# Kernel tuning notes

Measured on AMD Instinct MI355X. Metric: run time of the kernel, lower is better.

## Reference

```python
import jax, jax.numpy as jnp
import numpy as np
from jax import lax

D_MODEL = 768
N_LAYERS = 2
D_STATE = 16
D_CONV = 4
EXPAND = 2
D_INNER = EXPAND * D_MODEL
DT_RANK = 48  # ceil(768/16)
BETA = 0.9
ALPHA = 1.0
NS_STEPS = 1
EPS = 1e-5
BATCH = 2
SEQ = 512


def rmsnorm(x, w):
    return x * lax.rsqrt(jnp.mean(x * x, axis=-1, keepdims=True) + EPS) * w


def newton_schulz(X, steps):
    # Muon quintic Newton-Schulz orthogonalization on (B, D_INNER, D_STATE) matrices.
    a, b, c = 3.4445, -4.7750, 2.0315
    G = jnp.swapaxes(X, -1, -2)  # (B, N, Di) rows < cols
    G = G / (jnp.sqrt(jnp.sum(G * G, axis=(-2, -1), keepdims=True)) + 1e-7)
    for _ in range(steps):
        A = G @ jnp.swapaxes(G, -1, -2)  # (B, N, N)
        G = a * G + (b * A + c * (A @ A)) @ G
    return jnp.swapaxes(G, -1, -2)


def mamba_mixer(x, in_w, cw, cb, xp_w, dtp_w, dtp_b, A_log, Dp, out_w):
    B_, L, _ = x.shape
    xz = jnp.einsum('bld,ed->ble', x, in_w)  # (B, L, 2*Di)
    xi, z = jnp.split(xz, 2, axis=-1)
    # causal depthwise conv1d + silu
    xc = lax.conv_general_dilated(
        jnp.swapaxes(xi, 1, 2), cw, window_strides=(1,),
        padding=[(D_CONV - 1, 0)],
        dimension_numbers=('NCH', 'OIH', 'NCH'),
        feature_group_count=D_INNER)
    xc = jax.nn.silu(jnp.swapaxes(xc, 1, 2) + cb)  # (B, L, Di)
    x_dbl = jnp.einsum('bld,ed->ble', xc, xp_w)
    dt_lr = x_dbl[..., :DT_RANK]
    Bm = x_dbl[..., DT_RANK:DT_RANK + D_STATE]  # (B, L, N)
    Cm = x_dbl[..., DT_RANK + D_STATE:]         # (B, L, N)
    dt = jax.nn.softplus(jnp.einsum('blr,dr->bld', dt_lr, dtp_w) + dtp_b)
    A = -jnp.exp(A_log)  # (Di, N)
    dA = jnp.exp(dt[..., None] * A)                            # (B, L, Di, N)
    dBx = dt[..., None] * Bm[:, :, None, :] * xc[..., None]    # (B, L, Di, N)

    def step(carry, inp):
        h, v = carry
        dA_t, dBx_t, C_t = inp
        v = BETA * v + dBx_t                 # momentum velocity
        vu = newton_schulz(v, NS_STEPS)      # NS-orthogonalized update
        h = dA_t * h + ALPHA * vu
        y = jnp.einsum('bdn,bn->bd', h, C_t)
        return (h, v), y

    h0 = jnp.zeros((B_, D_INNER, D_STATE), x.dtype)
    v0 = jnp.zeros_like(h0)
    xs = (jnp.moveaxis(dA, 1, 0), jnp.moveaxis(dBx, 1, 0), jnp.moveaxis(Cm, 1, 0))
    _, ys = lax.scan(step, (h0, v0), xs)
    y = jnp.moveaxis(ys, 0, 1) + Dp * xc
    y = y * jax.nn.silu(z)
    return jnp.einsum('bld,ed->ble', y, out_w)


def forward(x, in_proj_w, conv_w, conv_b, x_proj_w, dt_proj_w, dt_proj_b,
            A_log, D, out_proj_w, norm_w, final_norm_w):
    for i in range(N_LAYERS):
        x = mamba_mixer(rmsnorm(x, norm_w[i]), in_proj_w[i], conv_w[i], conv_b[i],
                        x_proj_w[i], dt_proj_w[i], dt_proj_b[i], A_log[i], D[i],
                        out_proj_w[i]) + x
    return rmsnorm(x, final_norm_w)


def setup_inputs() -> dict:
    key = jax.random.key(0)
    ks = jax.random.split(key, 8)
    s = 0.02
    scale_out = s / np.sqrt(2 * N_LAYERS)
    A_init = jnp.broadcast_to(jnp.arange(1, D_STATE + 1, dtype=jnp.float32), (N_LAYERS, D_INNER, D_STATE))
    return {
        'x': jax.random.normal(ks[0], (BATCH, SEQ, D_MODEL), jnp.float32),
        'in_proj_w': jax.random.normal(ks[1], (N_LAYERS, 2 * D_INNER, D_MODEL), jnp.float32) * s,
        'conv_w': jax.random.normal(ks[2], (N_LAYERS, D_INNER, 1, D_CONV), jnp.float32) * 0.5,
        'conv_b': jnp.zeros((N_LAYERS, D_INNER), jnp.float32),
        'x_proj_w': jax.random.normal(ks[3], (N_LAYERS, DT_RANK + 2 * D_STATE, D_INNER), jnp.float32) * s,
        'dt_proj_w': jax.random.normal(ks[4], (N_LAYERS, D_INNER, DT_RANK), jnp.float32) * (DT_RANK ** -0.5),
        'dt_proj_b': jax.random.uniform(ks[5], (N_LAYERS, D_INNER), jnp.float32, -4.0, -2.0),
        'A_log': jnp.log(A_init),
        'D': jnp.ones((N_LAYERS, D_INNER), jnp.float32),
        'out_proj_w': jax.random.normal(ks[6], (N_LAYERS, D_MODEL, D_INNER), jnp.float32) * scale_out,
        'norm_w': jnp.ones((N_LAYERS, D_MODEL), jnp.float32),
        'final_norm_w': jnp.ones((D_MODEL,), jnp.float32),
    }


def reference(x, in_proj_w, conv_w, conv_b, x_proj_w, dt_proj_w, dt_proj_b,
              A_log, D, out_proj_w, norm_w, final_norm_w):
    return forward(x, in_proj_w, conv_w, conv_b, x_proj_w, dt_proj_w, dt_proj_b,
                   A_log, D, out_proj_w, norm_w, final_norm_w)
```

## Files before the change

### kernel.cpp

```cpp
#include <hip/hip_runtime.h>
#include <math.h>

#define DM   768
#define DI   1536
#define NDS  16
#define DTR  48
#define XDC  80
#define XPN  128
#define NB   2
#define SEQL 512
#define NT   (NB*SEQL)
#define CC   32
#define TT   16
#define BETA 0.9f
#define NSA  3.4445f
#define NSB  (-4.775f)
#define NSC  2.0315f
#define LOG2E 1.4426950408889634f
#define GKH  768
#define GKS  772
#define NCOL 32

typedef __attribute__((ext_vector_type(8))) short short8v;
typedef __attribute__((ext_vector_type(4))) float f32x4;

__device__ __forceinline__ float silu_(float x){ return x / (1.f + __expf(-x)); }
__device__ __forceinline__ unsigned short bfr(float x){
  unsigned u = __float_as_uint(x);
  return (unsigned short)((u + 0x7fffu + ((u>>16)&1u)) >> 16);
}
__device__ __forceinline__ void gl_lds16(const unsigned short* g, unsigned short* l){
  __builtin_amdgcn_global_load_lds((const __attribute__((address_space(1))) void*)g,
                                   (__attribute__((address_space(3))) void*)l, 16, 0, 0);
}

__global__ void rms_k(const float* __restrict__ X, const float* __restrict__ W,
                      unsigned short* __restrict__ O)
{
  const int g = blockIdx.x, tid = threadIdx.x;
  const float* xr = X + (size_t)g*DM;
  float x0 = xr[tid], x1 = xr[tid+256], x2 = xr[tid+512];
  float ss = x0*x0 + x1*x1 + x2*x2;
  #pragma unroll
  for (int m=1; m<=32; m<<=1) ss += __shfl_xor(ss, m);
  __shared__ float ws[4];
  if ((tid & 63) == 0) ws[tid>>6] = ss;
  __syncthreads();
  float sc = rsqrtf((ws[0]+ws[1]+ws[2]+ws[3])*(1.f/DM) + 1e-5f);
  unsigned short* o = O + (size_t)g*DM;
  o[tid]     = bfr(x0*sc*W[tid]);
  o[tid+256] = bfr(x1*sc*W[tid+256]);
  o[tid+512] = bfr(x2*sc*W[tid+512]);
}

__global__ void castall_k(const float* __restrict__ in_w, const float* __restrict__ out_w,
                          const float* __restrict__ xp_w,
                          unsigned short* __restrict__ wIn, unsigned short* __restrict__ wOut,
                          unsigned short* __restrict__ wXp)
{
  const int T0 = 2*2*DI*DM/4, T1 = 2*DM*DI/4, T2 = 2*XPN*DI/4;
  int i = blockIdx.x*256 + threadIdx.x;
  if (i < T0){
    float4 v = ((const float4*)in_w)[i];
    ushort4 o = { bfr(v.x), bfr(v.y), bfr(v.z), bfr(v.w) };
    ((ushort4*)wIn)[i] = o;
    return;
  }
  i -= T0;
  if (i < T1){
    float4 v = ((const float4*)out_w)[i];
    ushort4 o = { bfr(v.x), bfr(v.y), bfr(v.z), bfr(v.w) };
    ((ushort4*)wOut)[i] = o;
    return;
  }
  i -= T1;
  if (i < T2){
    const int l = i / (XPN*DI/4);
    const int r = i % (XPN*DI/4);
    const int row = r / (DI/4);
    const int k4 = r % (DI/4);
    ushort4 o = {0,0,0,0};
    if (row < XDC){
      float4 v = *(const float4*)(xp_w + ((size_t)l*XDC + row)*DI + k4*4);
      o.x = bfr(v.x); o.y = bfr(v.y); o.z = bfr(v.z); o.w = bfr(v.w);
    }
    ((ushort4*)wXp)[i] = o;
  }
}

__global__ __launch_bounds__(256) void gemm_mf(
    const unsigned short* __restrict__ Abf, int lda,
    const unsigned short* __restrict__ Bbf, int ldb,
    float* __restrict__ Out, float* __restrict__ Part,
    int M, int N, int K, int SK)
{
  __shared__ unsigned short As[128*32];
  __shared__ unsigned short Bs[128*32];
  const int tid  = threadIdx.x;
  const int wid  = tid >> 6, lane = tid & 63;
  const int bm   = blockIdx.y*128, bn = blockIdx.x*128;
  const int kc   = K/SK, kBeg = blockIdx.z*kc, kEnd = kBeg + kc;
  const int wr   = (wid>>1)*64, wc = (wid&1)*64;

  f32x4 acc[4][4];
  #pragma unroll
  for (int m=0;m<4;m++)
    #pragma unroll
    for (int n=0;n<4;n++) acc[m][n] = (f32x4){0.f,0.f,0.f,0.f};

  const int e0 = (wid*2)*512 + lane*8;
  const int e1 = e0 + 512;
  const int r0 = e0 >> 5, k0e = e0 & 31;
  const int r1 = e1 >> 5, k1e = e1 & 31;
  const unsigned short* Ag0 = Abf + (size_t)(bm + r0)*lda + k0e;
  const unsigned short* Ag1 = Abf + (size_t)(bm + r1)*lda + k1e;
  const unsigned short* Bg0 = Bbf + (size_t)(bn + r0)*ldb + k0e;
  const unsigned short* Bg1 = Bbf + (size_t)(bn + r1)*ldb + k1e;

  int aoff[4], boff[4];
  #pragma unroll
  for (int m=0;m<4;m++) aoff[m] = (wr + m*16 + (lane&15))*32 + (lane>>4)*8;
  #pragma unroll
  for (int n=0;n<4;n++) boff[n] = (wc + n*16 + (lane&15))*32 + (lane>>4)*8;

  for (int k0 = kBeg; k0 < kEnd; k0 += 32){
    gl_lds16(Ag0 + k0, As + e0);
    gl_lds16(Ag1 + k0, As + e1);
    gl_lds16(Bg0 + k0, Bs + e0);
    gl_lds16(Bg1 + k0, Bs + e1);
    __syncthreads();
    short8v af[4], bfv[4];
    #pragma unroll
    for (int m=0;m<4;m++) af[m]  = *(const short8v*)(As + aoff[m]);
    #pragma unroll
    for (int n=0;n<4;n++) bfv[n] = *(const short8v*)(Bs + boff[n]);
    #pragma unroll
    for (int m=0;m<4;m++)
      #pragma unroll
      for (int n=0;n<4;n++)
        acc[m][n] = __builtin_amdgcn_mfma_f32_16x16x32_bf16(af[m], bfv[n], acc[m][n], 0, 0, 0);
    __syncthreads();
  }

  #pragma unroll
  for (int m=0;m<4;m++){
    const int rowb = bm + wr + m*16 + (lane>>4)*4;
    #pragma unroll
    for (int n=0;n<4;n++){
      const int col = bn + wc + n*16 + (lane&15);
      #pragma unroll
      for (int r=0;r<4;r++){
        const int row = rowb + r;
        if (SK == 1) Out[(size_t)row*N + col] = acc[m][n][r];
        else         Part[(size_t)blockIdx.z*M*N + (size_t)row*N + col] = acc[m][n][r];
      }
    }
  }
}

__global__ void gemm64w(const float* __restrict__ A, int lda,
                        const float* __restrict__ Bw, int ldb,
                        float* __restrict__ Out, float* __restrict__ wOut,
                        const float* __restrict__ bias, const float* __restrict__ xc,
                        int M, int N, int K)
{
  __shared__ float As[16][64], Bs[16][64];
  const int tid = threadIdx.x;
  const int bm = blockIdx.y*64, bn = blockIdx.x*64;
  const int lr = tid>>2, lk = (tid&3)<<2;
  const int tx = tid&15, ty = tid>>4;
  float acc[4][4];
  #pragma unroll
  for (int i=0;i<4;i++)
    #pragma unroll
    for (int j=0;j<4;j++) acc[i][j] = 0.f;
  const float* Ap = A + (size_t)(bm+lr)*lda + lk;
  const float* Bp = Bw + (size_t)(bn+lr)*ldb + lk;
  for (int k0=0; k0<K; k0+=16){
    float4 a0 = *(const float4*)(Ap + k0);
    float4 b0 = *(const float4*)(Bp + k0);
    __syncthreads();
    As[lk+0][lr]=a0.x; As[lk+1][lr]=a0.y; As[lk+2][lr]=a0.z; As[lk+3][lr]=a0.w;
    Bs[lk+0][lr]=b0.x; Bs[lk+1][lr]=b0.y; Bs[lk+2][lr]=b0.z; Bs[lk+3][lr]=b0.w;
    __syncthreads();
    #pragma unroll
    for (int kk=0;kk<16;kk++){
      float a[4], b[4];
      *(float4*)a = *(const float4*)&As[kk][ty*4];
      *(float4*)b = *(const float4*)&Bs[kk][tx*4];
      #pragma unroll
      for (int i=0;i<4;i++)
        #pragma unroll
        for (int j=0;j<4;j++) acc[i][j] = fmaf(a[i], b[j], acc[i][j]);
    }
  }
  #pragma unroll
  for (int i=0;i<4;i++){
    const int row = bm + ty*4 + i;
    #pragma unroll
    for (int j=0;j<4;j++){
      const int col = bn + tx*4 + j;
      float vv = acc[i][j] + bias[col];
      vv = fmaxf(vv,0.f) + log1pf(__expf(-fabsf(vv)));
      Out[(size_t)row*N+col]  = vv;
      wOut[(size_t)row*N+col] = vv * xc[(size_t)row*N+col];
    }
  }
}

__global__ void reducepad_k(const float* __restrict__ Part, float* __restrict__ Out)
{
  const int i = blockIdx.x*256 + threadIdx.x;
  if (i >= NT*XDC) return;
  const int row = i / XDC, col = i % XDC;
  float s = 0.f;
  #pragma unroll
  for (int z=0; z<8; z++) s += Part[(size_t)z*NT*XPN + (size_t)row*XPN + col];
  Out[i] = s;
}

template<int MODE>
__global__ void reduce_rms_k(const float* __restrict__ Part, const float* __restrict__ res,
                             const float* __restrict__ W, float* __restrict__ nxt,
                             unsigned short* __restrict__ xnb, float* __restrict__ dout)
{
  const int g = blockIdx.x, tid = threadIdx.x;
  float s[3];
  #pragma unroll
  for (int j=0;j<3;j++){
    const int e = tid + j*256;
    float v = res[(size_t)g*DM + e];
    #pragma unroll
    for (int z=0;z<4;z++) v += Part[(size_t)z*NT*DM + (size_t)g*DM + e];
    s[j] = v;
    if (MODE==1) nxt[(size_t)g*DM + e] = v;
  }
  float ss = s[0]*s[0] + s[1]*s[1] + s[2]*s[2];
  #pragma unroll
  for (int m=1; m<=32; m<<=1) ss += __shfl_xor(ss, m);
  __shared__ float ws[4];
  if ((tid & 63) == 0) ws[tid>>6] = ss;
  __syncthreads();
  float sc = rsqrtf((ws[0]+ws[1]+ws[2]+ws[3])*(1.f/DM) + 1e-5f);
  #pragma unroll
  for (int j=0;j<3;j++){
    const int e = tid + j*256;
    if (MODE==1) xnb[(size_t)g*DM + e] = bfr(s[j]*sc*W[e]);
    else         dout[(size_t)g*DM + e] = s[j]*sc*W[e];
  }
}

__global__ void conv_k(const float* __restrict__ xz, const float* __restrict__ cw,
                       const float* __restrict__ cb, float* __restrict__ xc,
                       unsigned short* __restrict__ xc16)
{
  const int d = blockIdx.x*256 + threadIdx.x;
  const int g = blockIdx.y;
  const int b = g >> 9, t = g & (SEQL-1);
  float4 w4 = *(const float4*)(cw + (size_t)d*4);
  const float wk[4] = {w4.x, w4.y, w4.z, w4.w};
  const float* col = xz + ((size_t)b*SEQL)*(2*DI) + d;
  float acc = cb[d];
  #pragma unroll
  for (int k=0;k<4;k++){
    int tt = t - 3 + k;
    if (tt >= 0) acc = fmaf(wk[k], col[(size_t)tt*(2*DI)], acc);
  }
  const float r = silu_(acc);
  xc[(size_t)g*DI + d]   = r;
  xc16[(size_t)g*DI + d] = bfr(r);
}

__global__ void vagg_k(const float* __restrict__ dt, const float* __restrict__ wb,
                       const float* __restrict__ xdbl, float* __restrict__ Vagg,
                       float* __restrict__ cumdt)
{
  const int d = blockIdx.x*256 + threadIdx.x;
  const int c = blockIdx.y, b = blockIdx.z;
  float acc[16];
  #pragma unroll
  for (int n=0;n<16;n++) acc[n] = 0.f;
  float sdt = 0.f;
  for (int s=0;s<TT;s++){
    const int g = b*SEQL + c*TT + s;
    sdt += dt[(size_t)g*DI + d];
    cumdt[(size_t)g*DI + d] = sdt;
    const float w = wb[(size_t)g*DI + d];
    #pragma unroll
    for (int n=0;n<16;n++) acc[n] = fmaf(BETA, acc[n], w * xdbl[(size_t)g*XDC + 48 + n]);
  }
  const size_t base = ((size_t)(b*CC + c)*NDS)*DI + d;
  #pragma unroll
  for (int n=0;n<16;n++) Vagg[base + (size_t)n*DI] = acc[n];
}

__global__ void vcomb_k(float* V, float betaT)
{
  const int d = blockIdx.x*256 + threadIdx.x;
  const int n = blockIdx.y, b = blockIdx.z;
  const size_t stride = (size_t)NDS*DI;
  size_t idx = ((size_t)(b*CC)*NDS + n)*DI + d;
  float a = V[idx];
  float v = 0.f;
  for (int c=0;c<CC;c++){
    float an = (c+1<CC) ? V[idx+stride] : 0.f;
    V[idx] = v;
    v = fmaf(betaT, v, a);
    a = an; idx += stride;
  }
}

__global__ __launch_bounds__(256) void gram_k(
    const float* __restrict__ vst, const float* __restrict__ wb,
    const float* __restrict__ xdbl, float* __restrict__ Qg)
{
  const int c = blockIdx.x, b = blockIdx.y;
  const int tid = threadIdx.x;
  __shared__ float Xs[NCOL*GKS];
  __shared__ float Ms[NCOL][NCOL+1];
  __shared__ float sB[TT][16];
  __shared__ float Rm[16][17];

  const size_t vbase = ((size_t)(b*CC + c)*NDS)*DI;
  const size_t gbase = (size_t)(b*SEQL + c*TT);

  const bool active = tid < 216;
  const int tile = tid / 6, seg = tid % 6;
  int ti = 0, tj = 0;
  {
    int tt = tile;
    if (active){ while (tt >= 8 - ti){ tt -= 8 - ti; ti++; } tj = ti + tt; }
  }
  const int i0 = ti*4, j0 = tj*4;
  const int ks = seg*128;
  float acc[4][4];
  #pragma unroll
  for (int i=0;i<4;i++)
    #pragma unroll
    for (int j=0;j<4;j++) acc[i][j] = 0.f;

  for (int pass = 0; pass < 2; pass++){
    const int koff = pass * GKH;
    __syncthreads();
    #pragma unroll
    for (int q = 0; q < 24; q++){
      const int p = tid + q*256;
      const int col = p / 192;
      const int kk  = (p % 192) * 4;
      float4 xv;
      if (col < 16) xv = *(const float4*)(vst + vbase + (size_t)col*DI + koff + kk);
      else          xv = *(const float4*)(wb + (gbase + (col-16))*DI + koff + kk);
      *(float4*)(Xs + col*GKS + kk) = xv;
    }
    __syncthreads();
    if (active){
      for (int k4 = 0; k4 < 128; k4 += 4){
        float4 av[4], bv[4];
        #pragma unroll
        for (int r=0;r<4;r++) av[r] = *(const float4*)(Xs + (i0+r)*GKS + ks + k4);
        #pragma unroll
        for (int r=0;r<4;r++) bv[r] = *(const float4*)(Xs + (j0+r)*GKS + ks + k4);
        #pragma unroll
        for (int i=0;i<4;i++)
          #pragma unroll
          for (int j=0;j<4;j++){
            float s = fmaf(av[i].x, bv[j].x, acc[i][j]);
            s = fmaf(av[i].y, bv[j].y, s);
            s = fmaf(av[i].z, bv[j].z, s);
            acc[i][j] = fmaf(av[i].w, bv[j].w, s);
          }
      }
    }
  }
  __syncthreads();
  if (active){
    #pragma unroll
    for (int e=0;e<16;e++) Xs[(tile*16 + e)*6 + seg] = acc[e>>2][e&3];
  }
  { const int s = tid>>4, n = tid&15; sB[s][n] = xdbl[(gbase + s)*XDC + 48 + n]; }
  __syncthreads();
  for (int o = tid; o < 576; o += 256){
    const int tl = o >> 4, e = o & 15;
    int tt = tl, ti2 = 0;
    while (tt >= 8 - ti2){ tt -= 8 - ti2; ti2++; }
    const int tj2 = ti2 + tt;
    const int i = ti2*4 + (e>>2), j = tj2*4 + (e&3);
    float s = 0.f;
    #pragma unroll
    for (int sg=0; sg<6; sg++) s += Xs[o*6 + sg];
    Ms[i][j] = s; Ms[j][i] = s;
  }
  __syncthreads();

  const int i = tid >> 4, j = tid & 15;
  float Rreg = Ms[i][j];
  constexpr float PB[17] = {1.f, 0.9f, 0.81f, 0.729f, 0.6561f, 0.59049f,
                            0.531441f, 0.4782969f, 0.43046721f, 0.387420489f,
                            0.3486784401f, 0.31381059609f, 0.282429536481f,
                            0.2541865828329f, 0.22876792454961f, 0.205891132094649f,
                            0.1853020188851841f};
  const size_t qbase = ((size_t)(b*CC + c)*TT)*256;
  #pragma unroll
  for (int t=0;t<TT;t++){
    float p_i = PB[t]*Ms[i][16+t];
    float p_j = PB[t]*Ms[j][16+t];
    #pragma unroll
    for (int r=0;r<t;r++){
      const float gg = Ms[16+r][16+t];
      p_i = fmaf(PB[t-1-r]*gg, sB[r][i], p_i);
      p_j = fmaf(PB[t-1-r]*gg, sB[r][j], p_j);
    }
    const float bi = sB[t][i], bj = sB[t][j];
    const float gtt = Ms[16+t][16+t];
    Rreg = BETA*BETA*Rreg + BETA*(p_i*bj + bi*p_j) + gtt*bi*bj;
    Rm[i][j] = Rreg;
    __syncthreads();
    float tr = 0.f;
    #pragma unroll
    for (int k=0;k<16;k++) tr += Rm[k][k];
    const float nu = sqrtf(tr) + 1e-7f;
    const float inv_nu = 1.f/nu;
    const float inv2 = inv_nu*inv_nu;
    const float inv4 = inv2*inv2;
    float a2v = 0.f;
    #pragma unroll
    for (int k=0;k<16;k++) a2v = fmaf(Rm[i][k], Rm[k][j], a2v);
    float q = NSB*inv2*Rreg + NSC*inv4*a2v;
    if (i == j) q += NSA;
    Qg[qbase + t*256 + tid] = q * inv_nu;
    __syncthreads();
  }
}

__global__ __launch_bounds__(256) void apply_k(
    float* vh, const float* __restrict__ dt,
    const float* __restrict__ wb, const float* __restrict__ xdbl,
    const float* __restrict__ Qg, const float* __restrict__ A_log,
    float* __restrict__ ylocal)
{
  const int c = blockIdx.x, b = blockIdx.y, z = blockIdx.z;
  const int tid = threadIdx.x;
  const int d = z*256 + tid;
  __shared__ float sQ[TT*256];
  __shared__ float sBC[TT][32];

  const size_t qbase = ((size_t)(b*CC + c)*TT)*256;
  #pragma unroll
  for (int q=0;q<TT;q++) sQ[q*256 + tid] = Qg[qbase + q*256 + tid];
  #pragma unroll
  for (int rr=0; rr<2; rr++){
    const int p = tid + rr*256;
    sBC[p>>5][p&31] = xdbl[(size_t)((size_t)b*SEQL + c*TT + (p>>5))*XDC + 48 + (p&31)];
  }
  __syncthreads();

  float v[16], h[16], Ar[16];
  {
    float* vs = vh + ((size_t)(b*CC + c)*NDS)*DI + d;
    const float* arow = A_log + (size_t)d*NDS;
    #pragma unroll
    for (int n=0;n<16;n++){
      v[n] = vs[(size_t)n*DI];
      h[n] = 0.f;
      Ar[n] = -__expf(arow[n]) * LOG2E;
    }
  }

  for (int t=0;t<TT;t++){
    const size_t g = (size_t)(b*SEQL + c*TT + t);
    const float dtv = dt[g*DI + d];
    const float wv  = wb[g*DI + d];
    #pragma unroll
    for (int n=0;n<16;n++) v[n] = fmaf(BETA, v[n], wv*sBC[t][n]);
    float un[16];
    #pragma unroll
    for (int n=0;n<16;n++) un[n] = 0.f;
    const float* qt = sQ + t*256;
    #pragma unroll
    for (int k=0;k<16;k++){
      const float vk = v[k];
      const float4 q0 = *(const float4*)(qt + k*16);
      const float4 q1 = *(const float4*)(qt + k*16 + 4);
      const float4 q2 = *(const float4*)(qt + k*16 + 8);
      const float4 q3 = *(const float4*)(qt + k*16 + 12);
      un[0]=fmaf(vk,q0.x,un[0]); un[1]=fmaf(vk,q0.y,un[1]); un[2]=fmaf(vk,q0.z,un[2]); un[3]=fmaf(vk,q0.w,un[3]);
      un[4]=fmaf(vk,q1.x,un[4]); un[5]=fmaf(vk,q1.y,un[5]); un[6]=fmaf(vk,q1.z,un[6]); un[7]=fmaf(vk,q1.w,un[7]);
      un[8]=fmaf(vk,q2.x,un[8]); un[9]=fmaf(vk,q2.y,un[9]); un[10]=fmaf(vk,q2.z,un[10]); un[11]=fmaf(vk,q2.w,un[11]);
      un[12]=fmaf(vk,q3.x,un[12]); un[13]=fmaf(vk,q3.y,un[13]); un[14]=fmaf(vk,q3.z,un[14]); un[15]=fmaf(vk,q3.w,un[15]);
    }
    float y = 0.f;
    #pragma unroll
    for (int n=0;n<16;n++){
      const float e = exp2f(dtv*Ar[n]);
      h[n] = fmaf(e, h[n], un[n]);
      y = fmaf(h[n], sBC[t][16+n], y);
    }
    ylocal[g*DI + d] = y;
  }
  float* he = vh + ((size_t)(b*CC + c)*NDS)*DI + d;
  #pragma unroll
  for (int n=0;n<16;n++) he[(size_t)n*DI] = h[n];
}

__global__ void hcomb_k(float* H, const float* __restrict__ cumdt,
                        const float* __restrict__ A_log)
{
  const int d = blockIdx.x*256 + threadIdx.x;
  const int n = blockIdx.y, b = blockIdx.z;
  const float An = -__expf(A_log[(size_t)d*NDS + n]);
  const size_t stride = (size_t)NDS*DI;
  const size_t sstep = (size_t)TT*DI;
  size_t idx  = ((size_t)(b*CC)*NDS + n)*DI + d;
  size_t sidx = ((size_t)b*SEQL + TT-1)*DI + d;
  float a = H[idx];
  float sv = cumdt[sidx];
  float hv = 0.f;
  for (int c=0;c<CC;c++){
    float an = 0.f, sn = 0.f;
    if (c+1 < CC){ an = H[idx+stride]; sn = cumdt[sidx+sstep]; }
    H[idx] = hv;
    hv = fmaf(__expf(An * sv), hv, a);
    a = an; sv = sn;
    idx += stride; sidx += sstep;
  }
}

__global__ void yepi_k(const float* __restrict__ ylocal, const float* __restrict__ hst,
                       const float* __restrict__ cumdt, const float* __restrict__ xdbl,
                       const float* __restrict__ A_log, const float* __restrict__ Dv,
                       const float* __restrict__ xcp, const float* __restrict__ xz,
                       unsigned short* __restrict__ ybf)
{
  const int d = blockIdx.x*256 + threadIdx.x;
  const int g = blockIdx.y;
  const int b = g >> 9, t = g & (SEQL-1);
  const int c = t / TT;
  const float ddt = cumdt[(size_t)g*DI + d];
  const float* hs = hst + ((size_t)(b*CC + c)*NDS)*DI + d;
  const float* ar = A_log + (size_t)d*NDS;
  float corr = 0.f;
  #pragma unroll
  for (int n=0;n<16;n++){
    float An = -__expf(ar[n]);
    float Cn = xdbl[(size_t)g*XDC + 64 + n];
    corr = fmaf(hs[(size_t)n*DI] * __expf(An*ddt), Cn, corr);
  }
  float y = ylocal[(size_t)g*DI + d] + corr + Dv[d]*xcp[(size_t)g*DI + d];
  float z = xz[(size_t)g*(2*DI) + DI + d];
  ybf[(size_t)g*DI + d] = bfr(y * silu_(z));
}

extern "C" void kernel_launch(void* const* d_in, const int* in_sizes, int n_in,
                              void* d_out, int out_size, void* d_ws, size_t ws_size,
                              hipStream_t stream)
{
  (void)in_sizes; (void)n_in; (void)out_size; (void)ws_size;
  const float* x      = (const float*)d_in[0];
  const float* in_w   = (const float*)d_in[1];
  const float* conv_w = (const float*)d_in[2];
  const float* conv_b = (const float*)d_in[3];
  const float* xp_w   = (const float*)d_in[4];
  const float* dtp_w  = (const float*)d_in[5];
  const float* dtp_b  = (const float*)d_in[6];
  const float* A_log  = (const float*)d_in[7];
  const float* Dp     = (const float*)d_in[8];
  const float* out_w  = (const float*)d_in[9];
  const float* norm_w = (const float*)d_in[10];
  const float* fnorm  = (const float*)d_in[11];

  const float betaT = powf(BETA, (float)TT);

  float* w0 = (float*)d_ws; size_t off = 0;
  auto alloc = [&](size_t n)->float*{ float* p = w0 + off; off += (n + 63) & ~(size_t)63; return p; };
  float* xa     = alloc((size_t)NT*DM);
  float* bfA    = alloc((size_t)NT*DI/2);
  float* xz     = alloc((size_t)NT*2*DI);
  float* xcb    = alloc((size_t)NT*DI);
  float* xcbbF  = alloc((size_t)NT*DI/2);
  float* xdbl   = alloc((size_t)NT*XDC);
  float* dtb    = alloc((size_t)NT*DI);
  float* wbuf   = alloc((size_t)NT*DI);
  float* cumdt  = alloc((size_t)NT*DI);
  float* ylocal = alloc((size_t)NT*DI);
  float* Qg     = alloc((size_t)NB*CC*TT*256);
  float* big1   = alloc((size_t)NB*CC*NDS*DI);
  float* partb  = alloc((size_t)4*NT*DM);
  float* wInF   = alloc((size_t)2*2*DI*DM/2);
  float* wOutF  = alloc((size_t)2*DM*DI/2);
  float* wXpF   = alloc((size_t)2*XPN*DI/2);

  unsigned short* xnb  = (unsigned short*)bfA;
  unsigned short* ybf  = (unsigned short*)bfA;
  unsigned short* xcbb = (unsigned short*)xcbbF;
  unsigned short* wInb = (unsigned short*)wInF;
  unsigned short* wOutb= (unsigned short*)wOutF;
  unsigned short* wXpb = (unsigned short*)wXpF;

  {
    const int T0 = 2*2*DI*DM/4, T1 = 2*DM*DI/4, T2 = 2*XPN*DI/4;
    castall_k<<<dim3((T0+T1+T2+255)/256), dim3(256), 0, stream>>>(
        in_w, out_w, xp_w, wInb, wOutb, wXpb);
  }
  rms_k<<<dim3(NT), dim3(256), 0, stream>>>(x, norm_w, xnb);

  const float* xcur = x;
  for (int l=0; l<2; l++){
    const unsigned short* wIn_l  = wInb  + (size_t)l*2*DI*DM;
    const unsigned short* wOut_l = wOutb + (size_t)l*DM*DI;
    const unsigned short* wXp_l  = wXpb  + (size_t)l*XPN*DI;
    const float* cw_l  = conv_w + (size_t)l*DI*4;
    const float* cb_l  = conv_b + (size_t)l*DI;
    const float* dtw_l = dtp_w  + (size_t)l*DI*DTR;
    const float* dtbi  = dtp_b  + (size_t)l*DI;
    const float* al_l  = A_log  + (size_t)l*DI*NDS;
    const float* d_l   = Dp     + (size_t)l*DI;

    gemm_mf<<<dim3(2*DI/128, NT/128, 1), dim3(256), 0, stream>>>(
        xnb, DM, wIn_l, DM, xz, nullptr, NT, 2*DI, DM, 1);
    conv_k<<<dim3(DI/256, NT), dim3(256), 0, stream>>>(xz, cw_l, cb_l, xcb, xcbb);
    gemm_mf<<<dim3(XPN/128, NT/128, 8), dim3(256), 0, stream>>>(
        xcbb, DI, wXp_l, DI, nullptr, partb, NT, XPN, DI, 8);
    reducepad_k<<<dim3((NT*XDC+255)/256), dim3(256), 0, stream>>>(partb, xdbl);
    gemm64w<<<dim3(DI/64, NT/64, 1), dim3(256), 0, stream>>>(
        xdbl, XDC, dtw_l, DTR, dtb, wbuf, dtbi, xcb, NT, DI, DTR);
    vagg_k<<<dim3(DI/256, CC, NB), dim3(256), 0, stream>>>(dtb, wbuf, xdbl, big1, cumdt);
    vcomb_k<<<dim3(DI/256, NDS, NB), dim3(256), 0, stream>>>(big1, betaT);
    gram_k<<<dim3(CC, NB), dim3(256), 0, stream>>>(big1, wbuf, xdbl, Qg);
    apply_k<<<dim3(CC, NB, DI/256), dim3(256), 0, stream>>>(
        big1, dtb, wbuf, xdbl, Qg, al_l, ylocal);
    hcomb_k<<<dim3(DI/256, NDS, NB), dim3(256), 0, stream>>>(big1, cumdt, al_l);
    yepi_k<<<dim3(DI/256, NT), dim3(256), 0, stream>>>(
        ylocal, big1, cumdt, xdbl, al_l, d_l, xcb, xz, ybf);
    gemm_mf<<<dim3(DM/128, NT/128, 4), dim3(256), 0, stream>>>(
        ybf, DI, wOut_l, DI, nullptr, partb, NT, DM, DI, 4);
    if (l == 0)
      reduce_rms_k<1><<<dim3(NT), dim3(256), 0, stream>>>(
          partb, xcur, norm_w + DM, xa, xnb, nullptr);
    else
      reduce_rms_k<2><<<dim3(NT), dim3(256), 0, stream>>>(
          partb, xcur, fnorm, nullptr, nullptr, (float*)d_out);
    xcur = xa;
  }
}
```

Before: 441.9 us.

## Halve scan chunk length and fuse silu(z) into in_proj GEMM epilogue

Shrinks the chunked momentum-scan chunk from 16 to 8 timesteps (64 chunks), retuning the Gram kernel's tiling, thread mapping and shared-memory arrays to match, so per-chunk Gram and apply work is smaller and more parallel. Separately, the in_proj GEMM epilogue now writes x fp32 and silu(z) as bf16 into split buffers, so the z half no longer round-trips through the fp32 buffer and yepi reads half the bytes. The trade-offs are more chunks to combine sequentially in vcomb/hcomb, and slightly less precision on the gate.

```diff
diff --git a/kernel.cpp b/kernel.cpp
--- a/kernel.cpp
+++ b/kernel.cpp
@@ -10,8 +10,8 @@
 #define NB   2
 #define SEQL 512
 #define NT   (NB*SEQL)
-#define CC   32
-#define TT   16
+#define CC   64
+#define TT   8
 #define BETA 0.9f
 #define NSA  3.4445f
 #define NSB  (-4.775f)
@@ -19,7 +19,6 @@
 #define LOG2E 1.4426950408889634f
 #define GKH  768
 #define GKS  772
-#define NCOL 32
 
 typedef __attribute__((ext_vector_type(8))) short short8v;
 typedef __attribute__((ext_vector_type(4))) float f32x4;
@@ -28,6 +27,9 @@
 __device__ __forceinline__ unsigned short bfr(float x){
   unsigned u = __float_as_uint(x);
   return (unsigned short)((u + 0x7fffu + ((u>>16)&1u)) >> 16);
+}
+__device__ __forceinline__ float bf2f(unsigned short u){
+  return __uint_as_float(((unsigned)u) << 16);
 }
 __device__ __forceinline__ void gl_lds16(const unsigned short* g, unsigned short* l){
   __builtin_amdgcn_global_load_lds((const __attribute__((address_space(1))) void*)g,
@@ -88,10 +90,12 @@
   }
 }
 
+template<int EPI>
 __global__ __launch_bounds__(256) void gemm_mf(
     const unsigned short* __restrict__ Abf, int lda,
     const unsigned short* __restrict__ Bbf, int ldb,
     float* __restrict__ Out, float* __restrict__ Part,
+    unsigned short* __restrict__ OutZ,
     int M, int N, int K, int SK)
 {
   __shared__ unsigned short As[128*32];
@@ -151,8 +155,14 @@
       #pragma unroll
       for (int r=0;r<4;r++){
         const int row = rowb + r;
-        if (SK == 1) Out[(size_t)row*N + col] = acc[m][n][r];
-        else         Part[(size_t)blockIdx.z*M*N + (size_t)row*N + col] = acc[m][n][r];
+        const float vv = acc[m][n][r];
+        if (EPI==1){
+          if (col < DI) Out[(size_t)row*DI + col] = vv;
+          else          OutZ[(size_t)row*DI + col - DI] = bfr(silu_(vv));
+        } else {
+          if (SK == 1) Out[(size_t)row*N + col] = vv;
+          else         Part[(size_t)blockIdx.z*M*N + (size_t)row*N + col] = vv;
+        }
       }
     }
   }
@@ -250,7 +260,7 @@
   }
 }
 
-__global__ void conv_k(const float* __restrict__ xz, const float* __restrict__ cw,
+__global__ void conv_k(const float* __restrict__ xi, const float* __restrict__ cw,
                        const float* __restrict__ cb, float* __restrict__ xc,
                        unsigned short* __restrict__ xc16)
 {
@@ -259,12 +269,12 @@
   const int b = g >> 9, t = g & (SEQL-1);
   float4 w4 = *(const float4*)(cw + (size_t)d*4);
   const float wk[4] = {w4.x, w4.y, w4.z, w4.w};
-  const float* col = xz + ((size_t)b*SEQL)*(2*DI) + d;
+  const float* col = xi + ((size_t)b*SEQL)*DI + d;
   float acc = cb[d];
   #pragma unroll
   for (int k=0;k<4;k++){
     int tt = t - 3 + k;
-    if (tt >= 0) acc = fmaf(wk[k], col[(size_t)tt*(2*DI)], acc);
+    if (tt >= 0) acc = fmaf(wk[k], col[(size_t)tt*DI], acc);
   }
   const float r = silu_(acc);
   xc[(size_t)g*DI + d]   = r;
@@ -316,23 +326,23 @@
 {
   const int c = blockIdx.x, b = blockIdx.y;
   const int tid = threadIdx.x;
-  __shared__ float Xs[NCOL*GKS];
-  __shared__ float Ms[NCOL][NCOL+1];
-  __shared__ float sB[TT][16];
+  __shared__ float Xs[24*GKS];
+  __shared__ float Ms[24][25];
+  __shared__ float sB[8][16];
   __shared__ float Rm[16][17];
 
   const size_t vbase = ((size_t)(b*CC + c)*NDS)*DI;
   const size_t gbase = (size_t)(b*SEQL + c*TT);
 
-  const bool active = tid < 216;
-  const int tile = tid / 6, seg = tid % 6;
+  const bool active = tid < 252;
+  const int tile = tid / 12, seg = tid % 12;
   int ti = 0, tj = 0;
   {
     int tt = tile;
-    if (active){ while (tt >= 8 - ti){ tt -= 8 - ti; ti++; } tj = ti + tt; }
+    if (active){ while (tt >= 6 - ti){ tt -= 6 - ti; ti++; } tj = ti + tt; }
   }
   const int i0 = ti*4, j0 = tj*4;
-  const int ks = seg*128;
+  const int ks = seg*64;
   float acc[4][4];
   #pragma unroll
   for (int i=0;i<4;i++)
@@ -343,7 +353,7 @@
     const int koff = pass * GKH;
     __syncthreads();
     #pragma unroll
-    for (int q = 0; q < 24; q++){
+    for (int q = 0; q < 18; q++){
       const int p = tid + q*256;
       const int col = p / 192;
       const int kk  = (p % 192) * 4;
@@ -354,7 +364,7 @@
     }
     __syncthreads();
     if (active){
-      for (int k4 = 0; k4 < 128; k4 += 4){
+      for (int k4 = 0; k4 < 64; k4 += 4){
         float4 av[4], bv[4];
         #pragma unroll
         for (int r=0;r<4;r++) av[r] = *(const float4*)(Xs + (i0+r)*GKS + ks + k4);
@@ -375,30 +385,27 @@
   __syncthreads();
   if (active){
     #pragma unroll
-    for (int e=0;e<16;e++) Xs[(tile*16 + e)*6 + seg] = acc[e>>2][e&3];
-  }
-  { const int s = tid>>4, n = tid&15; sB[s][n] = xdbl[(gbase + s)*XDC + 48 + n]; }
+    for (int e=0;e<16;e++) Xs[(tile*16 + e)*12 + seg] = acc[e>>2][e&3];
+  }
+  if (tid < 128){ const int s = tid>>4, n = tid&15; sB[s][n] = xdbl[(gbase + s)*XDC + 48 + n]; }
   __syncthreads();
-  for (int o = tid; o < 576; o += 256){
+  for (int o = tid; o < 336; o += 256){
     const int tl = o >> 4, e = o & 15;
     int tt = tl, ti2 = 0;
-    while (tt >= 8 - ti2){ tt -= 8 - ti2; ti2++; }
+    while (tt >= 6 - ti2){ tt -= 6 - ti2; ti2++; }
     const int tj2 = ti2 + tt;
     const int i = ti2*4 + (e>>2), j = tj2*4 + (e&3);
     float s = 0.f;
     #pragma unroll
-    for (int sg=0; sg<6; sg++) s += Xs[o*6 + sg];
+    for (int sg=0; sg<12; sg++) s += Xs[o*12 + sg];
     Ms[i][j] = s; Ms[j][i] = s;
   }
   __syncthreads();
 
   const int i = tid >> 4, j = tid & 15;
   float Rreg = Ms[i][j];
-  constexpr float PB[17] = {1.f, 0.9f, 0.81f, 0.729f, 0.6561f, 0.59049f,
-                            0.531441f, 0.4782969f, 0.43046721f, 0.387420489f,
-                            0.3486784401f, 0.31381059609f, 0.282429536481f,
-                            0.2541865828329f, 0.22876792454961f, 0.205891132094649f,
-                            0.1853020188851841f};
+  constexpr float PB[9] = {1.f, 0.9f, 0.81f, 0.729f, 0.6561f, 0.59049f,
+                           0.531441f, 0.4782969f, 0.43046721f};
   const size_t qbase = ((size_t)(b*CC + c)*TT)*256;
   #pragma unroll
   for (int t=0;t<TT;t++){
@@ -447,10 +454,9 @@
   const size_t qbase = ((size_t)(b*CC + c)*TT)*256;
   #pragma unroll
   for (int q=0;q<TT;q++) sQ[q*256 + tid] = Qg[qbase + q*256 + tid];
-  #pragma unroll
-  for (int rr=0; rr<2; rr++){
-    const int p = tid + rr*256;
-    sBC[p>>5][p&31] = xdbl[(size_t)((size_t)b*SEQL + c*TT + (p>>5))*XDC + 48 + (p&31)];
+  {
+    const int s = tid >> 5, idx = tid & 31;
+    sBC[s][idx] = xdbl[(size_t)((size_t)b*SEQL + c*TT + s)*XDC + 48 + idx];
   }
   __syncthreads();
 
@@ -528,7 +534,7 @@
 __global__ void yepi_k(const float* __restrict__ ylocal, const float* __restrict__ hst,
                        const float* __restrict__ cumdt, const float* __restrict__ xdbl,
                        const float* __restrict__ A_log, const float* __restrict__ Dv,
-                       const float* __restrict__ xcp, const float* __restrict__ xz,
+                       const float* __restrict__ xcp, const unsigned short* __restrict__ szb,
                        unsigned short* __restrict__ ybf)
 {
   const int d = blockIdx.x*256 + threadIdx.x;
@@ -546,8 +552,8 @@
     corr = fmaf(hs[(size_t)n*DI] * __expf(An*ddt), Cn, corr);
   }
   float y = ylocal[(size_t)g*DI + d] + corr + Dv[d]*xcp[(size_t)g*DI + d];
-  float z = xz[(size_t)g*(2*DI) + DI + d];
-  ybf[(size_t)g*DI + d] = bfr(y * silu_(z));
+  const float sz = bf2f(szb[(size_t)g*DI + d]);
+  ybf[(size_t)g*DI + d] = bfr(y * sz);
 }
 
 extern "C" void kernel_launch(void* const* d_in, const int* in_sizes, int n_in,
@@ -574,7 +580,8 @@
   auto alloc = [&](size_t n)->float*{ float* p = w0 + off; off += (n + 63) & ~(size_t)63; return p; };
   float* xa     = alloc((size_t)NT*DM);
   float* bfA    = alloc((size_t)NT*DI/2);
-  float* xz     = alloc((size_t)NT*2*DI);
+  float* xi     = alloc((size_t)NT*DI);
+  float* szbF   = alloc((size_t)NT*DI/2);
   float* xcb    = alloc((size_t)NT*DI);
   float* xcbbF  = alloc((size_t)NT*DI/2);
   float* xdbl   = alloc((size_t)NT*XDC);
@@ -591,6 +598,7 @@
 
   unsigned short* xnb  = (unsigned short*)bfA;
   unsigned short* ybf  = (unsigned short*)bfA;
+  unsigned short* szb  = (unsigned short*)szbF;
   unsigned short* xcbb = (unsigned short*)xcbbF;
   unsigned short* wInb = (unsigned short*)wInF;
   unsigned short* wOutb= (unsigned short*)wOutF;
@@ -615,11 +623,11 @@
     const float* al_l  = A_log  + (size_t)l*DI*NDS;
     const float* d_l   = Dp     + (size_t)l*DI;
 
-    gemm_mf<<<dim3(2*DI/128, NT/128, 1), dim3(256), 0, stream>>>(
-        xnb, DM, wIn_l, DM, xz, nullptr, NT, 2*DI, DM, 1);
-    conv_k<<<dim3(DI/256, NT), dim3(256), 0, stream>>>(xz, cw_l, cb_l, xcb, xcbb);
-    gemm_mf<<<dim3(XPN/128, NT/128, 8), dim3(256), 0, stream>>>(
-        xcbb, DI, wXp_l, DI, nullptr, partb, NT, XPN, DI, 8);
+    gemm_mf<1><<<dim3(2*DI/128, NT/128, 1), dim3(256), 0, stream>>>(
+        xnb, DM, wIn_l, DM, xi, nullptr, szb, NT, 2*DI, DM, 1);
+    conv_k<<<dim3(DI/256, NT), dim3(256), 0, stream>>>(xi, cw_l, cb_l, xcb, xcbb);
+    gemm_mf<0><<<dim3(XPN/128, NT/128, 8), dim3(256), 0, stream>>>(
+        xcbb, DI, wXp_l, DI, nullptr, partb, nullptr, NT, XPN, DI, 8);
     reducepad_k<<<dim3((NT*XDC+255)/256), dim3(256), 0, stream>>>(partb, xdbl);
     gemm64w<<<dim3(DI/64, NT/64, 1), dim3(256), 0, stream>>>(
         xdbl, XDC, dtw_l, DTR, dtb, wbuf, dtbi, xcb, NT, DI, DTR);
@@ -630,9 +638,9 @@
         big1, dtb, wbuf, xdbl, Qg, al_l, ylocal);
     hcomb_k<<<dim3(DI/256, NDS, NB), dim3(256), 0, stream>>>(big1, cumdt, al_l);
     yepi_k<<<dim3(DI/256, NT), dim3(256), 0, stream>>>(
-        ylocal, big1, cumdt, xdbl, al_l, d_l, xcb, xz, ybf);
-    gemm_mf<<<dim3(DM/128, NT/128, 4), dim3(256), 0, stream>>>(
-        ybf, DI, wOut_l, DI, nullptr, partb, NT, DM, DI, 4);
+        ylocal, big1, cumdt, xdbl, al_l, d_l, xcb, szb, ybf);
+    gemm_mf<0><<<dim3(DM/128, NT/128, 4), dim3(256), 0, stream>>>(
+        ybf, DI, wOut_l, DI, nullptr, partb, nullptr, NT, DM, DI, 4);
     if (l == 0)
       reduce_rms_k<1><<<dim3(NT), dim3(256), 0, stream>>>(
           partb, xcur, norm_w + DM, xa, xnb, nullptr);
```

Result: faster. 431.1 us (-2.4%).
